# Performance work log

Hardware: AMD Instinct MI355X
Metric: run time of the kernel (lower is better)

Reference implementation:

```python
import jax, jax.numpy as jnp
import numpy as np

B, S, D, U = 16, 1024, 1024, 512  # batch, seq, d_model, cfc_units
LN_EPS = 1e-5


def setup_inputs() -> dict:
    key = jax.random.key(0)
    ks = jax.random.split(key, 12)
    sd_in = 1.0 / np.sqrt(D)
    sd_u = 1.0 / np.sqrt(U)
    return {
        "x": jax.random.normal(ks[0], (B, S, D), dtype=jnp.float32),
        "ln_gamma": jnp.ones((D,), jnp.float32),
        "ln_beta": jnp.zeros((D,), jnp.float32),
        # input_proj: Linear(D -> U)
        "w_in": jax.random.uniform(ks[1], (U, D), jnp.float32, -sd_in, sd_in),
        "b_in": jax.random.uniform(ks[2], (U,), jnp.float32, -sd_in, sd_in),
        # GRU weights (PyTorch layout: [3U, U], gate order r, z, n)
        "w_ih": jax.random.uniform(ks[3], (3 * U, U), jnp.float32, -sd_u, sd_u),
        "w_hh": jax.random.uniform(ks[4], (3 * U, U), jnp.float32, -sd_u, sd_u),
        "b_ih": jax.random.uniform(ks[5], (3 * U,), jnp.float32, -sd_u, sd_u),
        "b_hh": jax.random.uniform(ks[6], (3 * U,), jnp.float32, -sd_u, sd_u),
        # output_proj: Linear(U -> D)
        "w_out": jax.random.uniform(ks[7], (D, U), jnp.float32, -sd_u, sd_u),
        "b_out": jax.random.uniform(ks[8], (D,), jnp.float32, -sd_u, sd_u),
    }


def _layernorm(x, gamma, beta):
    mu = jnp.mean(x, axis=-1, keepdims=True)
    var = jnp.mean(jnp.square(x - mu), axis=-1, keepdims=True)
    return (x - mu) * jax.lax.rsqrt(var + LN_EPS) * gamma + beta


def reference(x, ln_gamma, ln_beta, w_in, b_in, w_ih, w_hh, b_ih, b_hh, w_out, b_out):
    residual = x
    xn = _layernorm(x, ln_gamma, ln_beta)                       # [B,S,D]
    u = jnp.einsum("bsd,ud->bsu", xn, w_in) + b_in              # [B,S,U]
    # precompute input-side gate activations for all timesteps (one big GEMM)
    gx = jnp.einsum("bsu,gu->bsg", u, w_ih) + b_ih              # [B,S,3U]

    def step(h, gx_t):                                          # gx_t [B,3U]
        gh = h @ w_hh.T + b_hh                                  # [B,3U]
        xr, xz, xn_ = jnp.split(gx_t, 3, axis=-1)
        hr, hz, hn = jnp.split(gh, 3, axis=-1)
        r = jax.nn.sigmoid(xr + hr)
        z = jax.nn.sigmoid(xz + hz)
        n = jnp.tanh(xn_ + r * hn)
        h_new = (1.0 - z) * n + z * h
        return h_new, h_new

    h0 = jnp.zeros((x.shape[0], w_hh.shape[1]), dtype=jnp.float32)
    h_last, ys = jax.lax.scan(step, h0, jnp.swapaxes(gx, 0, 1))  # ys [S,B,U]
    y = jnp.swapaxes(ys, 0, 1)                                   # [B,S,U]
    out = residual + (jnp.einsum("bsu,du->bsd", y, w_out) + b_out)
    return out, h_last
```

## Files before the change

kernel.cpp:

```cpp
#include <hip/hip_runtime.h>

typedef unsigned short ushort_t;
typedef unsigned int uint_t;
typedef __attribute__((ext_vector_type(8))) short bf16x8;
typedef __attribute__((ext_vector_type(4))) float f32x4;
typedef __attribute__((ext_vector_type(4))) unsigned int uintx4;

#define B_  16
#define S_  1024
#define D_  1024
#define U_  512
#define GU_ 1536

__device__ __forceinline__ ushort_t f2bf(float f) {
  union { float f; uint_t u; } v; v.f = f;
  uint_t r = v.u + 0x7fffu + ((v.u >> 16) & 1u);
  return (ushort_t)(r >> 16);
}
__device__ __forceinline__ float bf2f(ushort_t b) {
  union { uint_t u; float f; } v; v.u = ((uint_t)b) << 16; return v.f;
}

__global__ void cvt_f32_bf16(const float4* __restrict__ in, ushort4* __restrict__ out, int n4) {
  int i = blockIdx.x * blockDim.x + threadIdx.x;
  int stride = gridDim.x * blockDim.x;
  for (; i < n4; i += stride) {
    float4 f = in[i];
    ushort4 o; o.x = f2bf(f.x); o.y = f2bf(f.y); o.z = f2bf(f.z); o.w = f2bf(f.w);
    out[i] = o;
  }
}

__global__ __launch_bounds__(256) void ln_kernel(
    const float* __restrict__ x, const float* __restrict__ gamma,
    const float* __restrict__ beta, ushort_t* __restrict__ xn)
{
  int row = blockIdx.x;
  int t = threadIdx.x;
  const float* xr = x + (size_t)row * 1024;
  float4 v = *(const float4*)(xr + t * 4);
  float s = v.x + v.y + v.z + v.w;
  float ss = v.x * v.x + v.y * v.y + v.z * v.z + v.w * v.w;
#pragma unroll
  for (int o = 32; o > 0; o >>= 1) {
    s  += __shfl_down(s, o, 64);
    ss += __shfl_down(ss, o, 64);
  }
  __shared__ float red[2][4];
  __shared__ float mv[2];
  int wv = t >> 6, ln = t & 63;
  if (ln == 0) { red[0][wv] = s; red[1][wv] = ss; }
  __syncthreads();
  if (t == 0) {
    float S1 = red[0][0] + red[0][1] + red[0][2] + red[0][3];
    float S2 = red[1][0] + red[1][1] + red[1][2] + red[1][3];
    float mu = S1 * (1.f / 1024.f);
    float var = S2 * (1.f / 1024.f) - mu * mu;
    mv[0] = mu;
    mv[1] = rsqrtf(var + 1e-5f);
  }
  __syncthreads();
  float mu = mv[0], rs = mv[1];
  float4 gm = *(const float4*)(gamma + t * 4);
  float4 bt = *(const float4*)(beta + t * 4);
  ushort4 o;
  o.x = f2bf((v.x - mu) * rs * gm.x + bt.x);
  o.y = f2bf((v.y - mu) * rs * gm.y + bt.y);
  o.z = f2bf((v.z - mu) * rs * gm.z + bt.z);
  o.w = f2bf((v.w - mu) * rs * gm.w + bt.w);
  *(ushort4*)(xn + (size_t)row * 1024 + t * 4) = o;
}

template<int RES, int OBF>
__global__ __launch_bounds__(256, 2) void gemm_bt(
    const ushort_t* __restrict__ A, const ushort_t* __restrict__ Bw,
    const float* __restrict__ bias, const float* __restrict__ resid,
    void* __restrict__ Cout, int M, int N, int K)
{
  __shared__ ushort_t As[128][40];
  __shared__ ushort_t Bs[128][40];
  int bm = blockIdx.x, bn = blockIdx.y;
  int tid = threadIdx.x;
  int wave = tid >> 6, lane = tid & 63;
  int wm = wave >> 1, wn = wave & 1;
  int q = lane >> 4, l16 = lane & 15;
  f32x4 acc[4][4];
#pragma unroll
  for (int i = 0; i < 4; i++)
#pragma unroll
    for (int j = 0; j < 4; j++) acc[i][j] = (f32x4){0.f, 0.f, 0.f, 0.f};
  int r0 = tid >> 2, kc = tid & 3;
  const int nk = K >> 5;
  for (int it = 0; it < nk; ++it) {
#pragma unroll
    for (int h = 0; h < 2; ++h) {
      int r = r0 + h * 64;
      const uint4* pa = (const uint4*)(A + (size_t)(bm * 128 + r) * K + it * 32 + kc * 8);
      *(uint4*)&As[r][kc * 8] = *pa;
      const uint4* pb = (const uint4*)(Bw + (size_t)(bn * 128 + r) * K + it * 32 + kc * 8);
      *(uint4*)&Bs[r][kc * 8] = *pb;
    }
    __syncthreads();
    bf16x8 af[4], bfr[4];
#pragma unroll
    for (int i = 0; i < 4; i++) af[i]  = *(bf16x8*)&As[wm * 64 + i * 16 + l16][q * 8];
#pragma unroll
    for (int j = 0; j < 4; j++) bfr[j] = *(bf16x8*)&Bs[wn * 64 + j * 16 + l16][q * 8];
#pragma unroll
    for (int i = 0; i < 4; i++)
#pragma unroll
      for (int j = 0; j < 4; j++)
        acc[i][j] = __builtin_amdgcn_mfma_f32_16x16x32_bf16(af[i], bfr[j], acc[i][j], 0, 0, 0);
    __syncthreads();
  }
#pragma unroll
  for (int i = 0; i < 4; i++) {
#pragma unroll
    for (int j = 0; j < 4; j++) {
      int n = bn * 128 + wn * 64 + j * 16 + l16;
      float bv = bias[n];
#pragma unroll
      for (int rr = 0; rr < 4; rr++) {
        int m = bm * 128 + wm * 64 + i * 16 + q * 4 + rr;
        float v = acc[i][j][rr] + bv;
        if (RES) v += resid[(size_t)m * N + n];
        if (OBF) ((ushort_t*)Cout)[(size_t)m * N + n] = f2bf(v);
        else     ((float*)Cout)[(size_t)m * N + n] = v;
      }
    }
  }
}

__global__ __launch_bounds__(128, 1) void scan_kernel(
    const ushort_t* __restrict__ gx, const float* __restrict__ w_hh,
    const float* __restrict__ b_hh, uint_t* __restrict__ mdata,
    uint_t* __restrict__ mtag, ushort_t* __restrict__ y,
    float* __restrict__ h_last)
{
  extern __shared__ char smem[];
  ushort_t* wlds = (ushort_t*)smem;
  char* hshb = smem + 49152;

  const int m = blockIdx.x;
  const int c0 = m * 32;
  const int t = threadIdx.x;
  const int wv = t >> 6, lane = t & 63, q = lane >> 4, l16 = lane & 15;
  const int cl = (wv << 4) + l16;

  for (int idx = t; idx < 48 * 64; idx += 128) {
    int cc = idx >> 6, ln = idx & 63;
    int gi = cc >> 4, wv2 = (cc >> 3) & 1, ks = cc & 7;
    int n = c0 + (wv2 << 4) + (ln & 15);
    int k0 = (ks << 5) + ((ln >> 4) << 3);
    const float* src = w_hh + (size_t)(gi * 512 + n) * 512 + k0;
    float4 f0 = *(const float4*)src;
    float4 f1 = *(const float4*)(src + 4);
    uint4 pk;
    pk.x = (uint_t)f2bf(f0.x) | ((uint_t)f2bf(f0.y) << 16);
    pk.y = (uint_t)f2bf(f0.z) | ((uint_t)f2bf(f0.w) << 16);
    pk.z = (uint_t)f2bf(f1.x) | ((uint_t)f2bf(f1.y) << 16);
    pk.w = (uint_t)f2bf(f1.z) | ((uint_t)f2bf(f1.w) << 16);
    *(uint4*)(wlds + (size_t)cc * 512 + ln * 8) = pk;
  }
  bf16x8 wreg[3][8];
#pragma unroll
  for (int gi = 0; gi < 3; ++gi)
#pragma unroll
    for (int k8 = 0; k8 < 8; ++k8) {
      const float* src = w_hh + (size_t)(gi * 512 + c0 + cl) * 512 + (8 + k8) * 32 + q * 8;
      float4 f0 = *(const float4*)src;
      float4 f1 = *(const float4*)(src + 4);
      bf16x8 wf;
      wf[0] = (short)f2bf(f0.x); wf[1] = (short)f2bf(f0.y);
      wf[2] = (short)f2bf(f0.z); wf[3] = (short)f2bf(f0.w);
      wf[4] = (short)f2bf(f1.x); wf[5] = (short)f2bf(f1.y);
      wf[6] = (short)f2bf(f1.z); wf[7] = (short)f2bf(f1.w);
      wreg[gi][k8] = wf;
    }

  const float bhr = b_hh[c0 + cl];
  const float bhz = b_hh[512 + c0 + cl];
  const float bhn = b_hh[1024 + c0 + cl];
  float hcur[4] = {0.f, 0.f, 0.f, 0.f};

  ushort_t gxv[3][4];
#pragma unroll
  for (int g = 0; g < 3; ++g)
#pragma unroll
    for (int r = 0; r < 4; ++r)
      gxv[g][r] = gx[(size_t)(((q << 2) + r) * S_) * GU_ + g * 512 + c0 + cl];

  for (int i = t; i < 4096; i += 128) ((uint_t*)hshb)[i] = 0u;

  const int l64 = t & 63;
  for (int step = 0; step < S_; ++step) {
    if (step > 0) {
      const uint_t want = (uint_t)step;
      const int slot = (step - 1) & 1;
      const uint_t* tp = mtag + slot * 16 + (lane & 15);
      uint_t tv;
      do {
        asm volatile("global_load_dword %0, %1, off sc0 sc1"
                     : "=v"(tv) : "v"(tp) : "memory");
        asm volatile("s_waitcnt vmcnt(0)" ::: "memory");
      } while (!__all((int)(tv == want)));
      const uint_t* db = mdata + slot * 4096;
      uintx4 vals[8];
#pragma unroll
      for (int j = 0; j < 8; ++j) {
        const uint_t* p = db + j * 512 + t * 4;
        asm volatile("global_load_dwordx4 %0, %1, off sc0 sc1"
                     : "=v"(vals[j]) : "v"(p) : "memory");
      }
      asm volatile("s_waitcnt vmcnt(0)" ::: "memory");
#pragma unroll
      for (int j = 0; j < 8; ++j) {
        int b = 2 * j + wv;
        *(uint4*)(hshb + b * 1024 + ((l64 ^ (b & 7)) << 4)) = *(uint4*)&vals[j];
      }
    }
    __syncthreads();

    f32x4 acc[3] = {{0.f,0.f,0.f,0.f},{0.f,0.f,0.f,0.f},{0.f,0.f,0.f,0.f}};
#pragma unroll
    for (int ks = 0; ks < 16; ++ks) {
      bf16x8 hf = *(bf16x8*)(hshb + l16 * 1024 +
                             ((((ks << 2) + q) ^ (l16 & 7)) << 4));
#pragma unroll
      for (int gi = 0; gi < 3; ++gi) {
        bf16x8 wf;
        if (ks < 8) wf = *(bf16x8*)(wlds + (size_t)((gi * 2 + wv) * 8 + ks) * 512 + lane * 8);
        else        wf = wreg[gi][ks - 8];
        acc[gi] = __builtin_amdgcn_mfma_f32_16x16x32_bf16(hf, wf, acc[gi], 0, 0, 0);
      }
    }

    ushort_t hb16[4];
#pragma unroll
    for (int r = 0; r < 4; ++r) {
      float xr  = bf2f(gxv[0][r]);
      float xz  = bf2f(gxv[1][r]);
      float xnn = bf2f(gxv[2][r]);
      float rr = 1.f / (1.f + __expf(-(xr + acc[0][r] + bhr)));
      float zz = 1.f / (1.f + __expf(-(xz + acc[1][r] + bhz)));
      float na = xnn + rr * (acc[2][r] + bhn);
      float ng = 1.f - 2.f / (1.f + __expf(2.f * na));
      float hv = (1.f - zz) * ng + zz * hcur[r];
      hcur[r] = hv;
      hb16[r] = f2bf(hv);
    }

    if (step < S_ - 1) {
      const int oslot = step & 1;
#pragma unroll
      for (int r = 0; r < 4; ++r) {
        uint_t other = (uint_t)__shfl_xor((int)(uint_t)hb16[r], 1, 64);
        if ((lane & 1) == 0) {
          uint_t dw = ((uint_t)hb16[r]) | (other << 16);
          int b = (q << 2) + r;
          uint_t* pp = mdata + oslot * 4096 + b * 256 + ((c0 + cl) >> 1);
          asm volatile("global_store_dword %0, %1, off sc0 sc1"
                       :: "v"(pp), "v"(dw) : "memory");
        }
      }
      __syncthreads();
      if (t == 0) {
        uint_t tagv = (uint_t)(step + 1);
        uint_t* tp = mtag + oslot * 16 + m;
        asm volatile("global_store_dword %0, %1, off sc0 sc1"
                     :: "v"(tp), "v"(tagv) : "memory");
      }
    }

#pragma unroll
    for (int r = 0; r < 4; ++r)
      y[((size_t)((q << 2) + r) * S_ + step) * U_ + c0 + cl] = hb16[r];

    if (step + 1 < S_) {
#pragma unroll
      for (int g = 0; g < 3; ++g)
#pragma unroll
        for (int r = 0; r < 4; ++r)
          gxv[g][r] = gx[((size_t)((q << 2) + r) * S_ + step + 1) * GU_ +
                         g * 512 + c0 + cl];
    }
  }

#pragma unroll
  for (int r = 0; r < 4; ++r)
    h_last[((q << 2) + r) * 512 + c0 + cl] = hcur[r];
}

extern "C" void kernel_launch(void* const* d_in, const int* in_sizes, int n_in,
                              void* d_out, int out_size, void* d_ws, size_t ws_size,
                              hipStream_t stream) {
  const float* x     = (const float*)d_in[0];
  const float* ln_g  = (const float*)d_in[1];
  const float* ln_b  = (const float*)d_in[2];
  const float* w_in  = (const float*)d_in[3];
  const float* b_in  = (const float*)d_in[4];
  const float* w_ih  = (const float*)d_in[5];
  const float* w_hh  = (const float*)d_in[6];
  const float* b_ih  = (const float*)d_in[7];
  const float* b_hh  = (const float*)d_in[8];
  const float* w_out = (const float*)d_in[9];
  const float* b_out = (const float*)d_in[10];

  float* out = (float*)d_out;
  float* h_last = out + (size_t)B_ * S_ * D_;

  char* ws = (char*)d_ws;
  size_t off = 0;
  ushort_t* xn   = (ushort_t*)(ws + off); off += (size_t)B_ * S_ * D_ * 2;
  ushort_t* u    = (ushort_t*)(ws + off); off += (size_t)B_ * S_ * U_ * 2;
  ushort_t* gx   = (ushort_t*)(ws + off); off += (size_t)B_ * S_ * GU_ * 2;
  ushort_t* y    = (ushort_t*)(ws + off); off += (size_t)B_ * S_ * U_ * 2;
  ushort_t* winb = (ushort_t*)(ws + off); off += (size_t)U_ * D_ * 2;
  ushort_t* wihb = (ushort_t*)(ws + off); off += (size_t)GU_ * U_ * 2;
  ushort_t* woub = (ushort_t*)(ws + off); off += (size_t)D_ * U_ * 2;
  uint_t* mtag   = (uint_t*)(ws + off);   off += 256;
  uint_t* mdata  = (uint_t*)xn;

  cvt_f32_bf16<<<512, 256, 0, stream>>>((const float4*)w_in,  (ushort4*)winb, U_ * D_ / 4);
  cvt_f32_bf16<<<512, 256, 0, stream>>>((const float4*)w_ih,  (ushort4*)wihb, GU_ * U_ / 4);
  cvt_f32_bf16<<<512, 256, 0, stream>>>((const float4*)w_out, (ushort4*)woub, D_ * U_ / 4);

  ln_kernel<<<B_ * S_, 256, 0, stream>>>(x, ln_g, ln_b, xn);

  gemm_bt<0, 1><<<dim3(B_ * S_ / 128, U_ / 128), 256, 0, stream>>>(
      xn, winb, b_in, nullptr, u, B_ * S_, U_, D_);
  gemm_bt<0, 1><<<dim3(B_ * S_ / 128, GU_ / 128), 256, 0, stream>>>(
      u, wihb, b_ih, nullptr, gx, B_ * S_, GU_, U_);

  hipMemsetAsync(mtag, 0, 256, stream);

  (void)hipFuncSetAttribute(reinterpret_cast<const void*>(scan_kernel),
                            hipFuncAttributeMaxDynamicSharedMemorySize, 65536);
  scan_kernel<<<16, 128, 65536, stream>>>(gx, w_hh, b_hh, mdata, mtag, y, h_last);

  gemm_bt<1, 0><<<dim3(B_ * S_ / 128, D_ / 128), 256, 0, stream>>>(
      y, woub, b_out, x, out, B_ * S_, D_, U_);
}
```

Baseline: 3.072 ms.

## Embed step tags in exchanged h words and pipeline validated loads into MFMAs

Replaces the separate per-block tag flag plus data fetch with self-validating 32-bit words, each carrying one bf16 h value and the step tag in the upper half. Loads are issued in four groups and each group is validated and consumed by MFMAs directly from registers while later groups are in flight, removing the LDS staging of h, the flag-polling round trip and a per-step block barrier. All w_hh weights now sit in LDS (96KB) instead of half in registers. The cost is double the exchange traffic, a bounded retry loop that could exit silently after 4096 tries, and a larger LDS footprint.

```diff
diff --git a/kernel.cpp b/kernel.cpp
--- a/kernel.cpp
+++ b/kernel.cpp
@@ -131,15 +131,94 @@
   }
 }
 
+
+__device__ __forceinline__ const uint_t* slice_ptr(const uint_t* dbase, int ks) {
+  return dbase + ks * 32;
+}
+
+template<int KS0>
+__device__ __forceinline__ void issue_grp(uintx4 (&sv)[16][2], const uint_t* dbase) {
+#pragma unroll
+  for (int s = 0; s < 4; ++s) {
+    const uint_t* p = dbase + (KS0 + s) * 32;
+    asm volatile("global_load_dwordx4 %0, %2, off sc0 sc1\n\t"
+                 "global_load_dwordx4 %1, %2, off offset:16 sc0 sc1"
+                 : "=&v"(sv[KS0 + s][0]), "=&v"(sv[KS0 + s][1])
+                 : "v"(p) : "memory");
+  }
+}
+
+template<int KS0, int CNT>
+__device__ __forceinline__ void wait_grp(uintx4 (&sv)[16][2]) {
+  if constexpr (CNT == 0) {
+    asm volatile("s_waitcnt vmcnt(0)"
+        : "+v"(sv[KS0][0]), "+v"(sv[KS0][1]),
+          "+v"(sv[KS0 + 1][0]), "+v"(sv[KS0 + 1][1]),
+          "+v"(sv[KS0 + 2][0]), "+v"(sv[KS0 + 2][1]),
+          "+v"(sv[KS0 + 3][0]), "+v"(sv[KS0 + 3][1])
+        :: "memory");
+  } else {
+    asm volatile("s_waitcnt vmcnt(8)"
+        : "+v"(sv[KS0][0]), "+v"(sv[KS0][1]),
+          "+v"(sv[KS0 + 1][0]), "+v"(sv[KS0 + 1][1]),
+          "+v"(sv[KS0 + 2][0]), "+v"(sv[KS0 + 2][1]),
+          "+v"(sv[KS0 + 3][0]), "+v"(sv[KS0 + 3][1])
+        :: "memory");
+  }
+}
+
+template<int KS0>
+__device__ __forceinline__ int val_grp(uintx4 (&sv)[16][2], uint_t want) {
+  uint_t bad = 0;
+#pragma unroll
+  for (int s = 0; s < 4; ++s)
+#pragma unroll
+    for (int h = 0; h < 2; ++h)
+#pragma unroll
+      for (int d = 0; d < 4; ++d)
+        bad |= (sv[KS0 + s][h][d] >> 16) ^ want;
+  return __all(bad == 0);
+}
+
+template<int KS0, int CNT>
+__device__ __forceinline__ void get_grp(uintx4 (&sv)[16][2], const uint_t* dbase, uint_t want) {
+  wait_grp<KS0, CNT>(sv);
+  int ok = val_grp<KS0>(sv, want);
+  int tries = 0;
+  while (!ok && tries < 4096) {
+    issue_grp<KS0>(sv, dbase);
+    wait_grp<KS0, 0>(sv);
+    ok = val_grp<KS0>(sv, want);
+    ++tries;
+  }
+}
+
+template<int KS0>
+__device__ __forceinline__ void comp_grp(uintx4 (&sv)[16][2], const ushort_t* wlds,
+                                         int wv, int lane, f32x4 (&acc)[3]) {
+#pragma unroll
+  for (int s = 0; s < 4; ++s) {
+    union { bf16x8 h8; uint_t u[4]; } hu;
+    hu.u[0] = __builtin_amdgcn_perm(sv[KS0 + s][0][1], sv[KS0 + s][0][0], 0x05040100u);
+    hu.u[1] = __builtin_amdgcn_perm(sv[KS0 + s][0][3], sv[KS0 + s][0][2], 0x05040100u);
+    hu.u[2] = __builtin_amdgcn_perm(sv[KS0 + s][1][1], sv[KS0 + s][1][0], 0x05040100u);
+    hu.u[3] = __builtin_amdgcn_perm(sv[KS0 + s][1][3], sv[KS0 + s][1][2], 0x05040100u);
+#pragma unroll
+    for (int gi = 0; gi < 3; ++gi) {
+      bf16x8 wf = *(const bf16x8*)(wlds +
+          (size_t)(((gi * 2 + wv) * 16) + KS0 + s) * 512 + lane * 8);
+      acc[gi] = __builtin_amdgcn_mfma_f32_16x16x32_bf16(hu.h8, wf, acc[gi], 0, 0, 0);
+    }
+  }
+}
+
 __global__ __launch_bounds__(128, 1) void scan_kernel(
     const ushort_t* __restrict__ gx, const float* __restrict__ w_hh,
     const float* __restrict__ b_hh, uint_t* __restrict__ mdata,
-    uint_t* __restrict__ mtag, ushort_t* __restrict__ y,
-    float* __restrict__ h_last)
+    ushort_t* __restrict__ y, float* __restrict__ h_last)
 {
   extern __shared__ char smem[];
   ushort_t* wlds = (ushort_t*)smem;
-  char* hshb = smem + 49152;
 
   const int m = blockIdx.x;
   const int c0 = m * 32;
@@ -147,9 +226,9 @@
   const int wv = t >> 6, lane = t & 63, q = lane >> 4, l16 = lane & 15;
   const int cl = (wv << 4) + l16;
 
-  for (int idx = t; idx < 48 * 64; idx += 128) {
+  for (int idx = t; idx < 96 * 64; idx += 128) {
     int cc = idx >> 6, ln = idx & 63;
-    int gi = cc >> 4, wv2 = (cc >> 3) & 1, ks = cc & 7;
+    int gi = cc >> 5, wv2 = (cc >> 4) & 1, ks = cc & 15;
     int n = c0 + (wv2 << 4) + (ln & 15);
     int k0 = (ks << 5) + ((ln >> 4) << 3);
     const float* src = w_hh + (size_t)(gi * 512 + n) * 512 + k0;
@@ -162,21 +241,6 @@
     pk.w = (uint_t)f2bf(f1.z) | ((uint_t)f2bf(f1.w) << 16);
     *(uint4*)(wlds + (size_t)cc * 512 + ln * 8) = pk;
   }
-  bf16x8 wreg[3][8];
-#pragma unroll
-  for (int gi = 0; gi < 3; ++gi)
-#pragma unroll
-    for (int k8 = 0; k8 < 8; ++k8) {
-      const float* src = w_hh + (size_t)(gi * 512 + c0 + cl) * 512 + (8 + k8) * 32 + q * 8;
-      float4 f0 = *(const float4*)src;
-      float4 f1 = *(const float4*)(src + 4);
-      bf16x8 wf;
-      wf[0] = (short)f2bf(f0.x); wf[1] = (short)f2bf(f0.y);
-      wf[2] = (short)f2bf(f0.z); wf[3] = (short)f2bf(f0.w);
-      wf[4] = (short)f2bf(f1.x); wf[5] = (short)f2bf(f1.y);
-      wf[6] = (short)f2bf(f1.z); wf[7] = (short)f2bf(f1.w);
-      wreg[gi][k8] = wf;
-    }
 
   const float bhr = b_hh[c0 + cl];
   const float bhz = b_hh[512 + c0 + cl];
@@ -190,49 +254,28 @@
     for (int r = 0; r < 4; ++r)
       gxv[g][r] = gx[(size_t)(((q << 2) + r) * S_) * GU_ + g * 512 + c0 + cl];
 
-  for (int i = t; i < 4096; i += 128) ((uint_t*)hshb)[i] = 0u;
-
-  const int l64 = t & 63;
+  __syncthreads();
+
   for (int step = 0; step < S_; ++step) {
+    f32x4 acc[3] = {{0.f,0.f,0.f,0.f},{0.f,0.f,0.f,0.f},{0.f,0.f,0.f,0.f}};
+
     if (step > 0) {
       const uint_t want = (uint_t)step;
-      const int slot = (step - 1) & 1;
-      const uint_t* tp = mtag + slot * 16 + (lane & 15);
-      uint_t tv;
-      do {
-        asm volatile("global_load_dword %0, %1, off sc0 sc1"
-                     : "=v"(tv) : "v"(tp) : "memory");
-        asm volatile("s_waitcnt vmcnt(0)" ::: "memory");
-      } while (!__all((int)(tv == want)));
-      const uint_t* db = mdata + slot * 4096;
-      uintx4 vals[8];
-#pragma unroll
-      for (int j = 0; j < 8; ++j) {
-        const uint_t* p = db + j * 512 + t * 4;
-        asm volatile("global_load_dwordx4 %0, %1, off sc0 sc1"
-                     : "=v"(vals[j]) : "v"(p) : "memory");
-      }
-      asm volatile("s_waitcnt vmcnt(0)" ::: "memory");
-#pragma unroll
-      for (int j = 0; j < 8; ++j) {
-        int b = 2 * j + wv;
-        *(uint4*)(hshb + b * 1024 + ((l64 ^ (b & 7)) << 4)) = *(uint4*)&vals[j];
-      }
-    }
-    __syncthreads();
-
-    f32x4 acc[3] = {{0.f,0.f,0.f,0.f},{0.f,0.f,0.f,0.f},{0.f,0.f,0.f,0.f}};
-#pragma unroll
-    for (int ks = 0; ks < 16; ++ks) {
-      bf16x8 hf = *(bf16x8*)(hshb + l16 * 1024 +
-                             ((((ks << 2) + q) ^ (l16 & 7)) << 4));
-#pragma unroll
-      for (int gi = 0; gi < 3; ++gi) {
-        bf16x8 wf;
-        if (ks < 8) wf = *(bf16x8*)(wlds + (size_t)((gi * 2 + wv) * 8 + ks) * 512 + lane * 8);
-        else        wf = wreg[gi][ks - 8];
-        acc[gi] = __builtin_amdgcn_mfma_f32_16x16x32_bf16(hf, wf, acc[gi], 0, 0, 0);
-      }
+      const uint_t* dbase = mdata + ((size_t)((step - 1) & 1)) * 8192 +
+                            l16 * 512 + q * 8;
+      uintx4 sv[16][2];
+      issue_grp<0>(sv, dbase);
+      issue_grp<4>(sv, dbase);
+      get_grp<0, 8>(sv, dbase, want);
+      issue_grp<8>(sv, dbase);
+      comp_grp<0>(sv, wlds, wv, lane, acc);
+      get_grp<4, 8>(sv, dbase, want);
+      issue_grp<12>(sv, dbase);
+      comp_grp<4>(sv, wlds, wv, lane, acc);
+      get_grp<8, 8>(sv, dbase, want);
+      comp_grp<8>(sv, wlds, wv, lane, acc);
+      get_grp<12, 0>(sv, dbase, want);
+      comp_grp<12>(sv, wlds, wv, lane, acc);
     }
 
     ushort_t hb16[4];
@@ -252,23 +295,14 @@
 
     if (step < S_ - 1) {
       const int oslot = step & 1;
+      const uint_t tag = ((uint_t)(step + 1)) << 16;
+      uint_t* pb = mdata + oslot * 8192 + (c0 + cl);
 #pragma unroll
       for (int r = 0; r < 4; ++r) {
-        uint_t other = (uint_t)__shfl_xor((int)(uint_t)hb16[r], 1, 64);
-        if ((lane & 1) == 0) {
-          uint_t dw = ((uint_t)hb16[r]) | (other << 16);
-          int b = (q << 2) + r;
-          uint_t* pp = mdata + oslot * 4096 + b * 256 + ((c0 + cl) >> 1);
-          asm volatile("global_store_dword %0, %1, off sc0 sc1"
-                       :: "v"(pp), "v"(dw) : "memory");
-        }
-      }
-      __syncthreads();
-      if (t == 0) {
-        uint_t tagv = (uint_t)(step + 1);
-        uint_t* tp = mtag + oslot * 16 + m;
+        uint_t dw = (uint_t)hb16[r] | tag;
+        uint_t* pp = pb + ((q << 2) + r) * 512;
         asm volatile("global_store_dword %0, %1, off sc0 sc1"
-                     :: "v"(tp), "v"(tagv) : "memory");
+                     :: "v"(pp), "v"(dw) : "memory");
       }
     }
 
@@ -318,7 +352,6 @@
   ushort_t* winb = (ushort_t*)(ws + off); off += (size_t)U_ * D_ * 2;
   ushort_t* wihb = (ushort_t*)(ws + off); off += (size_t)GU_ * U_ * 2;
   ushort_t* woub = (ushort_t*)(ws + off); off += (size_t)D_ * U_ * 2;
-  uint_t* mtag   = (uint_t*)(ws + off);   off += 256;
   uint_t* mdata  = (uint_t*)xn;
 
   cvt_f32_bf16<<<512, 256, 0, stream>>>((const float4*)w_in,  (ushort4*)winb, U_ * D_ / 4);
@@ -332,11 +365,11 @@
   gemm_bt<0, 1><<<dim3(B_ * S_ / 128, GU_ / 128), 256, 0, stream>>>(
       u, wihb, b_ih, nullptr, gx, B_ * S_, GU_, U_);
 
-  hipMemsetAsync(mtag, 0, 256, stream);
+  hipMemsetAsync(mdata, 0, 65536, stream);
 
   (void)hipFuncSetAttribute(reinterpret_cast<const void*>(scan_kernel),
-                            hipFuncAttributeMaxDynamicSharedMemorySize, 65536);
-  scan_kernel<<<16, 128, 65536, stream>>>(gx, w_hh, b_hh, mdata, mtag, y, h_last);
+                            hipFuncAttributeMaxDynamicSharedMemorySize, 98304);
+  scan_kernel<<<16, 128, 98304, stream>>>(gx, w_hh, b_hh, mdata, y, h_last);
 
   gemm_bt<1, 0><<<dim3(B_ * S_ / 128, D_ / 128), 256, 0, stream>>>(
       y, woub, b_out, x, out, B_ * S_, D_, U_);
```

New measurement: 5.246 ms. 1.71x slower.

## Load hidden state straight into registers and use time-major gx/y layouts

Applied to the files above, without the earlier changes.

The scan kernel no longer stages the exchanged hidden state through shared memory. Each lane loads its MFMA operand fragments directly from the global exchange buffer, and per-fragment waitcnts let the MFMAs start while later loads are still in flight, which removes a __syncthreads and the LDS round trip from the serial step. The gx GEMM now writes rows in a time-major permuted order and the output GEMM reads y through the same permutation. This makes each step's gx reads and y writes contiguous, and the gx loads are issued at the top of the step. The cost is extra index arithmetic in the GEMMs and higher register use in the scan.

```diff
diff --git a/kernel.cpp b/kernel.cpp
--- a/kernel.cpp
+++ b/kernel.cpp
@@ -19,6 +19,10 @@
 }
 __device__ __forceinline__ float bf2f(ushort_t b) {
   union { uint_t u; float f; } v; v.u = ((uint_t)b) << 16; return v.f;
+}
+
+__device__ __forceinline__ int rp16(int m) {
+  return ((m & 1023) << 4) | (m >> 10);
 }
 
 __global__ void cvt_f32_bf16(const float4* __restrict__ in, ushort4* __restrict__ out, int n4) {
@@ -71,7 +75,7 @@
   *(ushort4*)(xn + (size_t)row * 1024 + t * 4) = o;
 }
 
-template<int RES, int OBF>
+template<int RES, int OBF, int APERM, int CPERM>
 __global__ __launch_bounds__(256, 2) void gemm_bt(
     const ushort_t* __restrict__ A, const ushort_t* __restrict__ Bw,
     const float* __restrict__ bias, const float* __restrict__ resid,
@@ -95,7 +99,9 @@
 #pragma unroll
     for (int h = 0; h < 2; ++h) {
       int r = r0 + h * 64;
-      const uint4* pa = (const uint4*)(A + (size_t)(bm * 128 + r) * K + it * 32 + kc * 8);
+      int arow = bm * 128 + r;
+      if (APERM) arow = rp16(arow);
+      const uint4* pa = (const uint4*)(A + (size_t)arow * K + it * 32 + kc * 8);
       *(uint4*)&As[r][kc * 8] = *pa;
       const uint4* pb = (const uint4*)(Bw + (size_t)(bn * 128 + r) * K + it * 32 + kc * 8);
       *(uint4*)&Bs[r][kc * 8] = *pb;
@@ -124,12 +130,30 @@
         int m = bm * 128 + wm * 64 + i * 16 + q * 4 + rr;
         float v = acc[i][j][rr] + bv;
         if (RES) v += resid[(size_t)m * N + n];
-        if (OBF) ((ushort_t*)Cout)[(size_t)m * N + n] = f2bf(v);
-        else     ((float*)Cout)[(size_t)m * N + n] = v;
+        int cm = CPERM ? rp16(m) : m;
+        if (OBF) ((ushort_t*)Cout)[(size_t)cm * N + n] = f2bf(v);
+        else     ((float*)Cout)[(size_t)cm * N + n] = v;
       }
     }
   }
 }
+
+
+#define SCAN_KS(ks, n)                                                         \
+  {                                                                            \
+    asm volatile("s_waitcnt vmcnt(" #n ")" : "+v"(sv[ks]) :: "memory");        \
+    bf16x8 hf = *(bf16x8*)&sv[ks];                                             \
+    _Pragma("unroll")                                                          \
+    for (int gi = 0; gi < 3; ++gi) {                                           \
+      bf16x8 wf;                                                               \
+      if ((ks) < 8)                                                            \
+        wf = *(const bf16x8*)(wlds +                                           \
+              (size_t)((gi * 2 + wv) * 8 + ((ks) & 7)) * 512 + lane * 8);      \
+      else                                                                     \
+        wf = wreg[gi][(ks) & 7];                                               \
+      acc[gi] = __builtin_amdgcn_mfma_f32_16x16x32_bf16(hf, wf, acc[gi], 0, 0, 0); \
+    }                                                                          \
+  }
 
 __global__ __launch_bounds__(128, 1) void scan_kernel(
     const ushort_t* __restrict__ gx, const float* __restrict__ w_hh,
@@ -139,7 +163,6 @@
 {
   extern __shared__ char smem[];
   ushort_t* wlds = (ushort_t*)smem;
-  char* hshb = smem + 49152;
 
   const int m = blockIdx.x;
   const int c0 = m * 32;
@@ -183,17 +206,18 @@
   const float bhn = b_hh[1024 + c0 + cl];
   float hcur[4] = {0.f, 0.f, 0.f, 0.f};
 
-  ushort_t gxv[3][4];
-#pragma unroll
-  for (int g = 0; g < 3; ++g)
-#pragma unroll
-    for (int r = 0; r < 4; ++r)
-      gxv[g][r] = gx[(size_t)(((q << 2) + r) * S_) * GU_ + g * 512 + c0 + cl];
-
-  for (int i = t; i < 4096; i += 128) ((uint_t*)hshb)[i] = 0u;
-
-  const int l64 = t & 63;
+  __syncthreads();
+
   for (int step = 0; step < S_; ++step) {
+    ushort_t gxv[3][4];
+#pragma unroll
+    for (int g = 0; g < 3; ++g)
+#pragma unroll
+      for (int r = 0; r < 4; ++r)
+        gxv[g][r] = gx[(size_t)(step * 16 + (q << 2) + r) * GU_ + g * 512 + c0 + cl];
+
+    f32x4 acc[3] = {{0.f,0.f,0.f,0.f},{0.f,0.f,0.f,0.f},{0.f,0.f,0.f,0.f}};
+
     if (step > 0) {
       const uint_t want = (uint_t)step;
       const int slot = (step - 1) & 1;
@@ -204,35 +228,18 @@
                      : "=v"(tv) : "v"(tp) : "memory");
         asm volatile("s_waitcnt vmcnt(0)" ::: "memory");
       } while (!__all((int)(tv == want)));
-      const uint_t* db = mdata + slot * 4096;
-      uintx4 vals[8];
-#pragma unroll
-      for (int j = 0; j < 8; ++j) {
-        const uint_t* p = db + j * 512 + t * 4;
+      const uint_t* dbase = mdata + (size_t)slot * 4096 + l16 * 256 + q * 4;
+      uintx4 sv[16];
+#pragma unroll
+      for (int ks = 0; ks < 16; ++ks) {
+        const uint_t* p = dbase + ks * 16;
         asm volatile("global_load_dwordx4 %0, %1, off sc0 sc1"
-                     : "=v"(vals[j]) : "v"(p) : "memory");
+                     : "=&v"(sv[ks]) : "v"(p) : "memory");
       }
-      asm volatile("s_waitcnt vmcnt(0)" ::: "memory");
-#pragma unroll
-      for (int j = 0; j < 8; ++j) {
-        int b = 2 * j + wv;
-        *(uint4*)(hshb + b * 1024 + ((l64 ^ (b & 7)) << 4)) = *(uint4*)&vals[j];
-      }
-    }
-    __syncthreads();
-
-    f32x4 acc[3] = {{0.f,0.f,0.f,0.f},{0.f,0.f,0.f,0.f},{0.f,0.f,0.f,0.f}};
-#pragma unroll
-    for (int ks = 0; ks < 16; ++ks) {
-      bf16x8 hf = *(bf16x8*)(hshb + l16 * 1024 +
-                             ((((ks << 2) + q) ^ (l16 & 7)) << 4));
-#pragma unroll
-      for (int gi = 0; gi < 3; ++gi) {
-        bf16x8 wf;
-        if (ks < 8) wf = *(bf16x8*)(wlds + (size_t)((gi * 2 + wv) * 8 + ks) * 512 + lane * 8);
-        else        wf = wreg[gi][ks - 8];
-        acc[gi] = __builtin_amdgcn_mfma_f32_16x16x32_bf16(hf, wf, acc[gi], 0, 0, 0);
-      }
+      SCAN_KS(0, 15)  SCAN_KS(1, 14)  SCAN_KS(2, 13)  SCAN_KS(3, 12)
+      SCAN_KS(4, 11)  SCAN_KS(5, 10)  SCAN_KS(6, 9)   SCAN_KS(7, 8)
+      SCAN_KS(8, 7)   SCAN_KS(9, 6)   SCAN_KS(10, 5)  SCAN_KS(11, 4)
+      SCAN_KS(12, 3)  SCAN_KS(13, 2)  SCAN_KS(14, 1)  SCAN_KS(15, 0)
     }
 
     ushort_t hb16[4];
@@ -249,6 +256,10 @@
       hcur[r] = hv;
       hb16[r] = f2bf(hv);
     }
+
+#pragma unroll
+    for (int r = 0; r < 4; ++r)
+      y[(size_t)(step * 16 + (q << 2) + r) * U_ + c0 + cl] = hb16[r];
 
     if (step < S_ - 1) {
       const int oslot = step & 1;
@@ -271,19 +282,6 @@
                      :: "v"(tp), "v"(tagv) : "memory");
       }
     }
-
-#pragma unroll
-    for (int r = 0; r < 4; ++r)
-      y[((size_t)((q << 2) + r) * S_ + step) * U_ + c0 + cl] = hb16[r];
-
-    if (step + 1 < S_) {
-#pragma unroll
-      for (int g = 0; g < 3; ++g)
-#pragma unroll
-        for (int r = 0; r < 4; ++r)
-          gxv[g][r] = gx[((size_t)((q << 2) + r) * S_ + step + 1) * GU_ +
-                         g * 512 + c0 + cl];
-    }
   }
 
 #pragma unroll
@@ -317,8 +315,8 @@
   ushort_t* y    = (ushort_t*)(ws + off); off += (size_t)B_ * S_ * U_ * 2;
   ushort_t* winb = (ushort_t*)(ws + off); off += (size_t)U_ * D_ * 2;
   ushort_t* wihb = (ushort_t*)(ws + off); off += (size_t)GU_ * U_ * 2;
+  uint_t* mtag   = (uint_t*)(ws + off);   off += 256;
   ushort_t* woub = (ushort_t*)(ws + off); off += (size_t)D_ * U_ * 2;
-  uint_t* mtag   = (uint_t*)(ws + off);   off += 256;
   uint_t* mdata  = (uint_t*)xn;
 
   cvt_f32_bf16<<<512, 256, 0, stream>>>((const float4*)w_in,  (ushort4*)winb, U_ * D_ / 4);
@@ -327,17 +325,17 @@
 
   ln_kernel<<<B_ * S_, 256, 0, stream>>>(x, ln_g, ln_b, xn);
 
-  gemm_bt<0, 1><<<dim3(B_ * S_ / 128, U_ / 128), 256, 0, stream>>>(
+  gemm_bt<0, 1, 0, 0><<<dim3(B_ * S_ / 128, U_ / 128), 256, 0, stream>>>(
       xn, winb, b_in, nullptr, u, B_ * S_, U_, D_);
-  gemm_bt<0, 1><<<dim3(B_ * S_ / 128, GU_ / 128), 256, 0, stream>>>(
+  gemm_bt<0, 1, 0, 1><<<dim3(B_ * S_ / 128, GU_ / 128), 256, 0, stream>>>(
       u, wihb, b_ih, nullptr, gx, B_ * S_, GU_, U_);
 
   hipMemsetAsync(mtag, 0, 256, stream);
 
   (void)hipFuncSetAttribute(reinterpret_cast<const void*>(scan_kernel),
-                            hipFuncAttributeMaxDynamicSharedMemorySize, 65536);
-  scan_kernel<<<16, 128, 65536, stream>>>(gx, w_hh, b_hh, mdata, mtag, y, h_last);
-
-  gemm_bt<1, 0><<<dim3(B_ * S_ / 128, D_ / 128), 256, 0, stream>>>(
+                            hipFuncAttributeMaxDynamicSharedMemorySize, 49152);
+  scan_kernel<<<16, 128, 49152, stream>>>(gx, w_hh, b_hh, mdata, mtag, y, h_last);
+
+  gemm_bt<1, 0, 1, 0><<<dim3(B_ * S_ / 128, D_ / 128), 256, 0, stream>>>(
       y, woub, b_out, x, out, B_ * S_, D_, U_);
 }
```

Result: slower. 3.150 ms (+2.5%).
